# Kernel tuning notes

Measured on AMD Instinct MI355X. Metric: run time of the kernel, lower is better.

## Reference

```python
import jax, jax.numpy as jnp
import numpy as np

N, E = 100000, 1600000
IN_C, OUT_C, H, EDGE_DIM = 128, 64, 2, 4
NEG_SLOPE = 0.2
LN_EPS = 1e-5


def setup_inputs() -> dict:
    key = jax.random.key(0)
    ks = jax.random.split(key, 12)
    s = 1.0 / np.sqrt(IN_C)
    inp = {
        "x": jax.random.normal(ks[0], (N, IN_C), jnp.float32),
        "edge_index": jax.random.randint(ks[1], (2, E), 0, N, jnp.int64),
        "edge_attr": jax.random.normal(ks[2], (E, EDGE_DIM), jnp.float32),
        "W": jax.random.normal(ks[3], (IN_C, H * OUT_C), jnp.float32) * s,
        "att_src": jax.random.normal(ks[4], (H, OUT_C), jnp.float32) * s,
        "att_dst": jax.random.normal(ks[5], (H, OUT_C), jnp.float32) * s,
        "W_edge": jax.random.normal(ks[6], (EDGE_DIM, H * OUT_C), jnp.float32) * 0.5,
        "att_edge": jax.random.normal(ks[7], (H, OUT_C), jnp.float32) * s,
        "bias": jnp.zeros((OUT_C,), jnp.float32),
        "gamma": jnp.ones((OUT_C,), jnp.float32),
        "beta": jnp.zeros((OUT_C,), jnp.float32),
    }
    return inp


def reference(x, edge_index, edge_attr, W, att_src, att_dst, W_edge, att_edge, bias, gamma, beta):
    n = x.shape[0]
    src, dst = edge_index[0], edge_index[1]
    # shared src/dst linear (PyG GATConv with single input tensor)
    h = (x @ W).reshape(n, H, OUT_C)                       # [N,H,C]
    a_src = jnp.einsum("nhc,hc->nh", h, att_src)          # [N,H]
    a_dst = jnp.einsum("nhc,hc->nh", h, att_dst)          # [N,H]
    e = (edge_attr @ W_edge).reshape(-1, H, OUT_C)         # [E,H,C]
    a_edge = jnp.einsum("ehc,hc->eh", e, att_edge)        # [E,H]
    alpha = jax.nn.leaky_relu(a_src[src] + a_dst[dst] + a_edge, NEG_SLOPE)  # [E,H]
    # segment softmax over edges grouped by destination node
    amax = jax.ops.segment_max(alpha, dst, num_segments=n)
    ex = jnp.exp(alpha - amax[dst])
    denom = jax.ops.segment_sum(ex, dst, num_segments=n)
    w = ex / (denom[dst] + 1e-16)                          # [E,H]
    msg = h[src] * w[:, :, None]                           # [E,H,C]
    out = jax.ops.segment_sum(msg, dst, num_segments=n)    # [N,H,C]
    out = out.mean(axis=1) + bias                          # concat=False -> head mean
    # LayerNorm + ReLU
    mu = out.mean(-1, keepdims=True)
    var = ((out - mu) ** 2).mean(-1, keepdims=True)
    out = (out - mu) * jax.lax.rsqrt(var + LN_EPS) * gamma + beta
    return jax.nn.relu(out)
```

## Files before the change

### kernel.cpp

```cpp
#include <hip/hip_runtime.h>
#include <hip/hip_fp16.h>
#include <math.h>

#define IN_C 128
#define HC   128
#define OUT_C 64
#define NEG_SLOPE 0.2f
#define LN_EPS 1e-5f
#define CHUNK 4096
#define BSH   8
#define BMSK  255
#define NBMAX 512
#define NB2MAX 1024

typedef __attribute__((ext_vector_type(8))) short bf16x8;
typedef __attribute__((ext_vector_type(4))) float f32x4;

__device__ inline unsigned bf16pack(float a, float b) {
    unsigned ua = __float_as_uint(a), ub = __float_as_uint(b);
    ua = (ua + 0x7fffu + ((ua >> 16) & 1u)) >> 16;
    ub = (ub + 0x7fffu + ((ub >> 16) & 1u)) >> 16;
    return ua | (ub << 16);
}

__global__ __launch_bounds__(256) void k_pre(const float* __restrict__ W,
                                             const float* __restrict__ W_edge,
                                             const float* __restrict__ att_edge,
                                             const int* __restrict__ ei_dst,
                                             unsigned short* __restrict__ WbfT,
                                             float* __restrict__ V,
                                             int* __restrict__ off,
                                             int E, int NB, int PB) {
    __shared__ int hist[NBMAX];
    int b = blockIdx.x, t = threadIdx.x;
    if (b < 8) {
        #pragma unroll
        for (int i = 0; i < 8; ++i) {
            int idx = b * 2048 + i * 256 + t;
            int k = idx >> 7, col = idx & 127;
            unsigned u = __float_as_uint(W[idx]);
            WbfT[col * 128 + k] =
                (unsigned short)((u + 0x7fffu + ((u >> 16) & 1u)) >> 16);
        }
        return;
    }
    if (b == 8) {
        if (t < 8) {
            int d = t >> 1, h = t & 1;
            float s = 0.f;
            for (int c = 0; c < 64; ++c)
                s += W_edge[d * HC + h * 64 + c] * att_edge[h * 64 + c];
            V[d * 2 + h] = s;
        }
        return;
    }
    int pb = b - 9;
    for (int i = t; i < NB; i += 256) hist[i] = 0;
    __syncthreads();
    int base = pb * CHUNK;
    int lim = E - base; if (lim > CHUNK) lim = CHUNK;
    if (lim == CHUNK) {
        #pragma unroll
        for (int u = 0; u < 4; ++u) {
            int4 v = *(const int4*)&ei_dst[base + u * 1024 + t * 4];
            atomicAdd(&hist[v.x >> BSH], 1);
            atomicAdd(&hist[v.y >> BSH], 1);
            atomicAdd(&hist[v.z >> BSH], 1);
            atomicAdd(&hist[v.w >> BSH], 1);
        }
    } else {
        for (int i = t; i < lim; i += 256)
            atomicAdd(&hist[ei_dst[base + i] >> BSH], 1);
    }
    __syncthreads();
    for (int i = t; i < NB; i += 256)
        off[(size_t)i * PB + pb] = hist[i];
}

__global__ __launch_bounds__(256) void k_mid(const float* __restrict__ x,
                                             const unsigned short* __restrict__ WbfT,
                                             const float* __restrict__ attS,
                                             const float* __restrict__ attD,
                                             unsigned* __restrict__ hb,
                                             float* __restrict__ a_src,
                                             float* __restrict__ a_dst, int M,
                                             int* __restrict__ off,
                                             int* __restrict__ bsum,
                                             int nS, int GB) {
    __shared__ unsigned xb[64 * 64];
    const int t = threadIdx.x;
    const int bid = blockIdx.x;

    if (bid >= GB) {
        int* sm = (int*)xb;
        int blk = bid - GB;
        int base = blk * 1024 + t * 4;
        int v0 = 0, v1 = 0, v2 = 0, v3 = 0;
        if (base + 0 < nS) v0 = off[base + 0];
        if (base + 1 < nS) v1 = off[base + 1];
        if (base + 2 < nS) v2 = off[base + 2];
        if (base + 3 < nS) v3 = off[base + 3];
        int s = v0 + v1 + v2 + v3;
        sm[t] = s;
        __syncthreads();
        for (int o = 1; o < 256; o <<= 1) {
            int u = (t >= o) ? sm[t - o] : 0;
            __syncthreads();
            sm[t] += u;
            __syncthreads();
        }
        int excl = sm[t] - s;
        if (base + 0 < nS) off[base + 0] = excl;
        if (base + 1 < nS) off[base + 1] = excl + v0;
        if (base + 2 < nS) off[base + 2] = excl + v0 + v1;
        if (base + 3 < nS) off[base + 3] = excl + v0 + v1 + v2;
        if (t == 255) bsum[blk] = sm[255];
        return;
    }

    const int brow = bid * 64;
    const float4* x4 = (const float4*)x;
    #pragma unroll
    for (int i = 0; i < 8; ++i) {
        int idx = i * 256 + t;
        int row = idx >> 5, c4 = idx & 31;
        float4 v = make_float4(0.f, 0.f, 0.f, 0.f);
        if (brow + row < M) v = x4[(size_t)(brow + row) * 32 + c4];
        unsigned lo = bf16pack(v.x, v.y), hi = bf16pack(v.z, v.w);
        int byte = row * 256 + ((c4 * 8) ^ ((row & 7) << 4));
        *(uint2*)((char*)xb + byte) = make_uint2(lo, hi);
    }
    __syncthreads();

    const int w = t >> 6, lane = t & 63;
    const int col = lane & 15, qr = lane >> 4;
    f32x4 acc[8];
    #pragma unroll
    for (int ct = 0; ct < 8; ++ct) acc[ct] = (f32x4){0.f, 0.f, 0.f, 0.f};

    const int arow = w * 16 + col;
    #pragma unroll
    for (int ks = 0; ks < 4; ++ks) {
        int abyte = arow * 256 + ((ks * 64 + qr * 16) ^ ((arow & 7) << 4));
        bf16x8 af = *(const bf16x8*)((const char*)xb + abyte);
        #pragma unroll
        for (int ct = 0; ct < 8; ++ct) {
            bf16x8 bfr = *(const bf16x8*)&WbfT[(size_t)(ct * 16 + col) * 128 + ks * 32 + qr * 8];
            acc[ct] = __builtin_amdgcn_mfma_f32_16x16x32_bf16(af, bfr, acc[ct], 0, 0, 0);
        }
    }

    float pS0[4], pS1[4], pD0[4], pD1[4];
    #pragma unroll
    for (int r = 0; r < 4; ++r) { pS0[r] = pS1[r] = pD0[r] = pD1[r] = 0.f; }
    #pragma unroll
    for (int ct = 0; ct < 8; ++ct) {
        float s = attS[ct * 16 + col], d = attD[ct * 16 + col];
        #pragma unroll
        for (int r = 0; r < 4; ++r) {
            float a = acc[ct][r];
            if (ct < 4) { pS0[r] += a * s; pD0[r] += a * d; }
            else        { pS1[r] += a * s; pD1[r] += a * d; }
        }
    }
    #pragma unroll
    for (int m = 1; m < 16; m <<= 1) {
        #pragma unroll
        for (int r = 0; r < 4; ++r) {
            pS0[r] += __shfl_xor(pS0[r], m);
            pS1[r] += __shfl_xor(pS1[r], m);
            pD0[r] += __shfl_xor(pD0[r], m);
            pD1[r] += __shfl_xor(pD1[r], m);
        }
    }
    #pragma unroll
    for (int r = 0; r < 4; ++r) {
        int grow = brow + w * 16 + qr * 4 + r;
        if (grow < M) {
            if (col == 0) {
                a_src[2 * grow + 0] = pS0[r];
                a_src[2 * grow + 1] = pS1[r];
                a_dst[2 * grow + 0] = pD0[r];
                a_dst[2 * grow + 1] = pD1[r];
            }
            #pragma unroll
            for (int ct = 0; ct < 4; ++ct)
                hb[(size_t)grow * 64 + ct * 16 + col] =
                    bf16pack(acc[ct][r], acc[ct + 4][r]);
        }
    }
}

__device__ inline void scan_bsum(const int* __restrict__ bsum, int nb2,
                                 int* bs, int* sm, int t) {
    int v0 = (4 * t + 0 < nb2) ? bsum[4 * t + 0] : 0;
    int v1 = (4 * t + 1 < nb2) ? bsum[4 * t + 1] : 0;
    int v2 = (4 * t + 2 < nb2) ? bsum[4 * t + 2] : 0;
    int v3 = (4 * t + 3 < nb2) ? bsum[4 * t + 3] : 0;
    int s = v0 + v1 + v2 + v3;
    sm[t] = s;
    __syncthreads();
    for (int o = 1; o < 256; o <<= 1) {
        int u = (t >= o) ? sm[t - o] : 0;
        __syncthreads();
        sm[t] += u;
        __syncthreads();
    }
    int excl = sm[t] - s;
    bs[4 * t + 0] = excl;
    bs[4 * t + 1] = excl + v0;
    bs[4 * t + 2] = excl + v0 + v1;
    bs[4 * t + 3] = excl + v0 + v1 + v2;
    __syncthreads();
}

__global__ __launch_bounds__(256) void k_part(const int* __restrict__ ei,
                                              const float* __restrict__ ea,
                                              const float* __restrict__ V,
                                              const float* __restrict__ a_src,
                                              const float* __restrict__ a_dst,
                                              const int* __restrict__ off,
                                              const int* __restrict__ bsum,
                                              int* __restrict__ bsum2,
                                              uint2* __restrict__ pA,
                                              int E, int NB, int PB, int nb2) {
    __shared__ int cur[NBMAX];
    __shared__ int bs[NB2MAX];
    __shared__ int sm[256];
    int pb = blockIdx.x, t = threadIdx.x;

    scan_bsum(bsum, nb2, bs, sm, t);
    if (pb == 0)
        for (int i = t; i < nb2; i += 256) bsum2[i] = bs[i];

    for (int i = t; i < NB; i += 256) {
        size_t oi = (size_t)i * PB + pb;
        cur[i] = off[oi] + bs[(int)(oi >> 10)];
    }
    __syncthreads();
    float v0 = V[0], v1 = V[1], v2 = V[2], v3 = V[3];
    float v4 = V[4], v5 = V[5], v6 = V[6], v7 = V[7];
    int base = pb * CHUNK;
    int lim = E - base; if (lim > CHUNK) lim = CHUNK;

    if (lim == CHUNK) {
        #pragma unroll
        for (int h = 0; h < 2; ++h) {
            int e0 = base + h * 2048 + t;
            int sA[8], dA[8];
            #pragma unroll
            for (int k = 0; k < 8; ++k) {
                sA[k] = ei[e0 + k * 256];
                dA[k] = ei[E + e0 + k * 256];
            }
            float4 aA[8];
            #pragma unroll
            for (int k = 0; k < 8; ++k) aA[k] = ((const float4*)ea)[e0 + k * 256];
            float2 asA[8], adA[8];
            #pragma unroll
            for (int k = 0; k < 8; ++k) {
                asA[k] = ((const float2*)a_src)[sA[k]];
                adA[k] = ((const float2*)a_dst)[dA[k]];
            }
            #pragma unroll
            for (int k = 0; k < 8; ++k) {
                float ae0 = aA[k].x * v0 + aA[k].y * v2 + aA[k].z * v4 + aA[k].w * v6;
                float ae1 = aA[k].x * v1 + aA[k].y * v3 + aA[k].z * v5 + aA[k].w * v7;
                float al0 = asA[k].x + adA[k].x + ae0;
                al0 = al0 > 0.f ? al0 : NEG_SLOPE * al0;
                float al1 = asA[k].y + adA[k].y + ae1;
                al1 = al1 > 0.f ? al1 : NEG_SLOPE * al1;
                __half2 hx = __floats2half2_rn(__expf(al0), __expf(al1));
                int slot = atomicAdd(&cur[dA[k] >> BSH], 1);
                pA[slot] = make_uint2((unsigned)sA[k] | ((unsigned)(dA[k] & BMSK) << 17),
                                      *reinterpret_cast<unsigned*>(&hx));
            }
        }
    } else {
        for (int i = t; i < lim; i += 256) {
            int e = base + i;
            int s = ei[e], d = ei[E + e];
            float4 a = ((const float4*)ea)[e];
            float ae0 = a.x * v0 + a.y * v2 + a.z * v4 + a.w * v6;
            float ae1 = a.x * v1 + a.y * v3 + a.z * v5 + a.w * v7;
            float2 as = ((const float2*)a_src)[s];
            float2 ad = ((const float2*)a_dst)[d];
            float al0 = as.x + ad.x + ae0; al0 = al0 > 0.f ? al0 : NEG_SLOPE * al0;
            float al1 = as.y + ad.y + ae1; al1 = al1 > 0.f ? al1 : NEG_SLOPE * al1;
            __half2 hx = __floats2half2_rn(__expf(al0), __expf(al1));
            int slot = atomicAdd(&cur[d >> BSH], 1);
            pA[slot] = make_uint2((unsigned)s | ((unsigned)(d & BMSK) << 17),
                                  *reinterpret_cast<unsigned*>(&hx));
        }
    }
}

__global__ __launch_bounds__(256) void k_csr(const uint2* __restrict__ pA,
                                             const int* __restrict__ off,
                                             const int* __restrict__ bsum2,
                                             int* __restrict__ rowptr,
                                             uint2* __restrict__ payload,
                                             int M, int E, int NB, int PB) {
    __shared__ int cnt[256];
    __shared__ int sc[256];
    __shared__ int cur[256];
    int b = blockIdx.x, t = threadIdx.x;
    int n0 = b << BSH;
    int nloc = M - n0; if (nloc > 256) nloc = 256;

    size_t o0 = (size_t)b * PB;
    int s0 = off[o0] + bsum2[(int)(o0 >> 10)];
    int s1 = E;
    if (b + 1 < NB) {
        size_t o1 = (size_t)(b + 1) * PB;
        s1 = off[o1] + bsum2[(int)(o1 >> 10)];
    }
    cnt[t] = 0;
    __syncthreads();

    for (int i = s0 + t; i < s1; i += 256)
        atomicAdd(&cnt[(pA[i].x >> 17) & BMSK], 1);
    __syncthreads();
    int c = cnt[t];
    sc[t] = c;
    __syncthreads();
    for (int o = 1; o < 256; o <<= 1) {
        int u = (t >= o) ? sc[t - o] : 0;
        __syncthreads();
        sc[t] += u;
        __syncthreads();
    }
    {
        int base = s0 + sc[t] - c;
        cur[t] = base;
        if (t < nloc) rowptr[n0 + t] = base;
    }
    if (b == NB - 1 && t == 0) rowptr[M] = E;
    __syncthreads();
    for (int i = s0 + t; i < s1; i += 256) {
        uint2 p = pA[i];
        int dl = (p.x >> 17) & BMSK;
        int pos = atomicAdd(&cur[dl], 1);
        payload[pos] = make_uint2(p.x & 0x1FFFF, p.y);
    }
}

__global__ __launch_bounds__(256) void k_gather(const uint2* __restrict__ payload,
                                                const int* __restrict__ rowptr,
                                                const unsigned* __restrict__ hb,
                                                const float* __restrict__ bias,
                                                const float* __restrict__ gamma,
                                                const float* __restrict__ beta,
                                                float* __restrict__ out, int M) {
    __shared__ uint2 stg[4][64];
    int w = threadIdx.x >> 6, lane = threadIdx.x & 63;
    int n = blockIdx.x * 4 + w;
    if (n >= M) return;
    int beg = rowptr[n], end = rowptr[n + 1];
    float acc0 = 0.f, acc1 = 0.f, pe0 = 0.f, pe1 = 0.f;

    for (int base = beg; base < end; base += 64) {
        int cnt = end - base; if (cnt > 64) cnt = 64;
        uint2 p = make_uint2(0u, 0u);
        if (lane < cnt) p = payload[base + lane];
        stg[w][lane] = p;
        {
            __half2 he = *reinterpret_cast<__half2*>(&p.y);
            pe0 += __low2float(he);
            pe1 += __high2float(he);
        }
        int j = 0;
        for (; j + 8 <= cnt; j += 8) {
            uint2 q0 = stg[w][j + 0], q1 = stg[w][j + 1];
            uint2 q2 = stg[w][j + 2], q3 = stg[w][j + 3];
            uint2 q4 = stg[w][j + 4], q5 = stg[w][j + 5];
            uint2 q6 = stg[w][j + 6], q7 = stg[w][j + 7];
            int s0 = __builtin_amdgcn_readfirstlane((int)q0.x);
            int s1 = __builtin_amdgcn_readfirstlane((int)q1.x);
            int s2 = __builtin_amdgcn_readfirstlane((int)q2.x);
            int s3 = __builtin_amdgcn_readfirstlane((int)q3.x);
            int s4 = __builtin_amdgcn_readfirstlane((int)q4.x);
            int s5 = __builtin_amdgcn_readfirstlane((int)q5.x);
            int s6 = __builtin_amdgcn_readfirstlane((int)q6.x);
            int s7 = __builtin_amdgcn_readfirstlane((int)q7.x);
            unsigned h0 = (hb + (size_t)s0 * 64)[lane];
            unsigned h1 = (hb + (size_t)s1 * 64)[lane];
            unsigned h2 = (hb + (size_t)s2 * 64)[lane];
            unsigned h3 = (hb + (size_t)s3 * 64)[lane];
            unsigned h4 = (hb + (size_t)s4 * 64)[lane];
            unsigned h5 = (hb + (size_t)s5 * 64)[lane];
            unsigned h6 = (hb + (size_t)s6 * 64)[lane];
            unsigned h7 = (hb + (size_t)s7 * 64)[lane];
            __half2 e0 = *reinterpret_cast<__half2*>(&q0.y);
            __half2 e1 = *reinterpret_cast<__half2*>(&q1.y);
            __half2 e2 = *reinterpret_cast<__half2*>(&q2.y);
            __half2 e3 = *reinterpret_cast<__half2*>(&q3.y);
            __half2 e4 = *reinterpret_cast<__half2*>(&q4.y);
            __half2 e5 = *reinterpret_cast<__half2*>(&q5.y);
            __half2 e6 = *reinterpret_cast<__half2*>(&q6.y);
            __half2 e7 = *reinterpret_cast<__half2*>(&q7.y);
            acc0 += __low2float(e0)  * __uint_as_float(h0 << 16);
            acc1 += __high2float(e0) * __uint_as_float(h0 & 0xffff0000u);
            acc0 += __low2float(e1)  * __uint_as_float(h1 << 16);
            acc1 += __high2float(e1) * __uint_as_float(h1 & 0xffff0000u);
            acc0 += __low2float(e2)  * __uint_as_float(h2 << 16);
            acc1 += __high2float(e2) * __uint_as_float(h2 & 0xffff0000u);
            acc0 += __low2float(e3)  * __uint_as_float(h3 << 16);
            acc1 += __high2float(e3) * __uint_as_float(h3 & 0xffff0000u);
            acc0 += __low2float(e4)  * __uint_as_float(h4 << 16);
            acc1 += __high2float(e4) * __uint_as_float(h4 & 0xffff0000u);
            acc0 += __low2float(e5)  * __uint_as_float(h5 << 16);
            acc1 += __high2float(e5) * __uint_as_float(h5 & 0xffff0000u);
            acc0 += __low2float(e6)  * __uint_as_float(h6 << 16);
            acc1 += __high2float(e6) * __uint_as_float(h6 & 0xffff0000u);
            acc0 += __low2float(e7)  * __uint_as_float(h7 << 16);
            acc1 += __high2float(e7) * __uint_as_float(h7 & 0xffff0000u);
        }
        for (; j + 4 <= cnt; j += 4) {
            uint2 q0 = stg[w][j + 0], q1 = stg[w][j + 1];
            uint2 q2 = stg[w][j + 2], q3 = stg[w][j + 3];
            int s0 = __builtin_amdgcn_readfirstlane((int)q0.x);
            int s1 = __builtin_amdgcn_readfirstlane((int)q1.x);
            int s2 = __builtin_amdgcn_readfirstlane((int)q2.x);
            int s3 = __builtin_amdgcn_readfirstlane((int)q3.x);
            unsigned h0 = (hb + (size_t)s0 * 64)[lane];
            unsigned h1 = (hb + (size_t)s1 * 64)[lane];
            unsigned h2 = (hb + (size_t)s2 * 64)[lane];
            unsigned h3 = (hb + (size_t)s3 * 64)[lane];
            __half2 e0 = *reinterpret_cast<__half2*>(&q0.y);
            __half2 e1 = *reinterpret_cast<__half2*>(&q1.y);
            __half2 e2 = *reinterpret_cast<__half2*>(&q2.y);
            __half2 e3 = *reinterpret_cast<__half2*>(&q3.y);
            acc0 += __low2float(e0)  * __uint_as_float(h0 << 16);
            acc1 += __high2float(e0) * __uint_as_float(h0 & 0xffff0000u);
            acc0 += __low2float(e1)  * __uint_as_float(h1 << 16);
            acc1 += __high2float(e1) * __uint_as_float(h1 & 0xffff0000u);
            acc0 += __low2float(e2)  * __uint_as_float(h2 << 16);
            acc1 += __high2float(e2) * __uint_as_float(h2 & 0xffff0000u);
            acc0 += __low2float(e3)  * __uint_as_float(h3 << 16);
            acc1 += __high2float(e3) * __uint_as_float(h3 & 0xffff0000u);
        }
        for (; j < cnt; ++j) {
            uint2 q0 = stg[w][j];
            int s0 = __builtin_amdgcn_readfirstlane((int)q0.x);
            unsigned h0 = (hb + (size_t)s0 * 64)[lane];
            __half2 e0 = *reinterpret_cast<__half2*>(&q0.y);
            acc0 += __low2float(e0)  * __uint_as_float(h0 << 16);
            acc1 += __high2float(e0) * __uint_as_float(h0 & 0xffff0000u);
        }
    }

    float d0 = pe0, d1 = pe1;
    #pragma unroll
    for (int m = 32; m; m >>= 1) {
        d0 += __shfl_xor(d0, m);
        d1 += __shfl_xor(d1, m);
    }

    float o = 0.5f * (acc0 / (d0 + 1e-16f) + acc1 / (d1 + 1e-16f)) + bias[lane];
    float mu = o;
    #pragma unroll
    for (int m = 32; m; m >>= 1) mu += __shfl_xor(mu, m);
    mu *= (1.f / 64.f);
    float c = o - mu;
    float v = c * c;
    #pragma unroll
    for (int m = 32; m; m >>= 1) v += __shfl_xor(v, m);
    v *= (1.f / 64.f);
    float y = c * rsqrtf(v + LN_EPS) * gamma[lane] + beta[lane];
    out[(size_t)n * OUT_C + lane] = fmaxf(y, 0.f);
}

extern "C" void kernel_launch(void* const* d_in, const int* in_sizes, int n_in,
                              void* d_out, int out_size, void* d_ws, size_t ws_size,
                              hipStream_t stream) {
    const float* x     = (const float*)d_in[0];
    const int*   ei    = (const int*)d_in[1];
    const float* ea    = (const float*)d_in[2];
    const float* W     = (const float*)d_in[3];
    const float* attS  = (const float*)d_in[4];
    const float* attD  = (const float*)d_in[5];
    const float* We    = (const float*)d_in[6];
    const float* attE  = (const float*)d_in[7];
    const float* bias  = (const float*)d_in[8];
    const float* gamma = (const float*)d_in[9];
    const float* beta  = (const float*)d_in[10];

    const int M  = in_sizes[0] / IN_C;
    const int E  = in_sizes[1] / 2;
    const int NB = (M + BMSK) >> BSH;
    const int PB = (E + CHUNK - 1) / CHUNK;
    const int nS = NB * PB;
    const int nb2 = (nS + 1023) / 1024;
    const int GB = (M + 63) / 64;

    char* ws = (char*)d_ws;
    size_t woff = 0;
    auto alloc = [&](size_t bytes) -> void* {
        void* p = ws + woff;
        woff += (bytes + 255) & ~(size_t)255;
        return p;
    };
    unsigned*       hb     = (unsigned*)      alloc((size_t)M * 64 * 4);
    float*          a_src  = (float*)         alloc((size_t)M * 2 * 4);
    float*          a_dst  = (float*)         alloc((size_t)M * 2 * 4);
    int*            off    = (int*)           alloc((size_t)nS * 4);
    int*            bsum   = (int*)           alloc((size_t)nb2 * 4);
    int*            bsum2  = (int*)           alloc((size_t)nb2 * 4);
    int*            rowptr = (int*)           alloc((size_t)(M + 1) * 4);
    uint2*          pA     = (uint2*)         alloc((size_t)E * 8);
    uint2*          payload= (uint2*)         alloc((size_t)E * 8);
    unsigned short* WbfT   = (unsigned short*)alloc(128 * 128 * 2);
    float*          V      = (float*)         alloc(32);

    k_pre<<<9 + PB, 256, 0, stream>>>(W, We, attE, ei + E, WbfT, V, off, E, NB, PB);
    k_mid<<<GB + nb2, 256, 0, stream>>>(x, WbfT, attS, attD, hb, a_src, a_dst, M,
                                        off, bsum, nS, GB);
    k_part<<<PB, 256, 0, stream>>>(ei, ea, V, a_src, a_dst, off, bsum, bsum2,
                                   pA, E, NB, PB, nb2);
    k_csr<<<NB, 256, 0, stream>>>(pA, off, bsum2, rowptr, payload, M, E, NB, PB);
    k_gather<<<(M + 3) / 4, 256, 0, stream>>>(payload, rowptr, hb, bias, gamma, beta,
                                              (float*)d_out, M);
}
```

Measured before the change: 159.1 us.

## Overlap edge partitioning with node GEMM by deferring attention logits to CSR pass

Splits the offset scan into its own kernel and fuses the node projection GEMM with the edge partition pass into one interleaved launch, with one in five blocks partitioning edges. This lets the two independent workloads run concurrently. The attention logit and exp computation moves into the CSR build, which stores the edge term as half in the payload and gathers a_src there. The cost is an extra random gather of a_src in k_csr, a separate scan launch, and precision loss from storing the pre-activation edge logit in fp16.

Result: faster. 144.1 us (-9.5%).

```diff
diff --git a/kernel.cpp b/kernel.cpp
--- a/kernel.cpp
+++ b/kernel.cpp
@@ -77,48 +77,133 @@
         off[(size_t)i * PB + pb] = hist[i];
 }
 
-__global__ __launch_bounds__(256) void k_mid(const float* __restrict__ x,
-                                             const unsigned short* __restrict__ WbfT,
-                                             const float* __restrict__ attS,
-                                             const float* __restrict__ attD,
-                                             unsigned* __restrict__ hb,
-                                             float* __restrict__ a_src,
-                                             float* __restrict__ a_dst, int M,
-                                             int* __restrict__ off,
-                                             int* __restrict__ bsum,
-                                             int nS, int GB) {
+__global__ __launch_bounds__(256) void k_scan(int* __restrict__ off,
+                                              int* __restrict__ bsum, int nS) {
+    __shared__ int sm[256];
+    int t = threadIdx.x;
+    int base = blockIdx.x * 1024 + t * 4;
+    int v0 = 0, v1 = 0, v2 = 0, v3 = 0;
+    if (base + 0 < nS) v0 = off[base + 0];
+    if (base + 1 < nS) v1 = off[base + 1];
+    if (base + 2 < nS) v2 = off[base + 2];
+    if (base + 3 < nS) v3 = off[base + 3];
+    int s = v0 + v1 + v2 + v3;
+    sm[t] = s;
+    __syncthreads();
+    for (int o = 1; o < 256; o <<= 1) {
+        int u = (t >= o) ? sm[t - o] : 0;
+        __syncthreads();
+        sm[t] += u;
+        __syncthreads();
+    }
+    int excl = sm[t] - s;
+    if (base + 0 < nS) off[base + 0] = excl;
+    if (base + 1 < nS) off[base + 1] = excl + v0;
+    if (base + 2 < nS) off[base + 2] = excl + v0 + v1;
+    if (base + 3 < nS) off[base + 3] = excl + v0 + v1 + v2;
+    if (t == 255) bsum[blockIdx.x] = sm[255];
+}
+
+__device__ inline void scan_bsum(const int* __restrict__ bsum, int nb2,
+                                 int* bs, int* sm, int t) {
+    int v0 = (4 * t + 0 < nb2) ? bsum[4 * t + 0] : 0;
+    int v1 = (4 * t + 1 < nb2) ? bsum[4 * t + 1] : 0;
+    int v2 = (4 * t + 2 < nb2) ? bsum[4 * t + 2] : 0;
+    int v3 = (4 * t + 3 < nb2) ? bsum[4 * t + 3] : 0;
+    int s = v0 + v1 + v2 + v3;
+    sm[t] = s;
+    __syncthreads();
+    for (int o = 1; o < 256; o <<= 1) {
+        int u = (t >= o) ? sm[t - o] : 0;
+        __syncthreads();
+        sm[t] += u;
+        __syncthreads();
+    }
+    int excl = sm[t] - s;
+    bs[4 * t + 0] = excl;
+    bs[4 * t + 1] = excl + v0;
+    bs[4 * t + 2] = excl + v0 + v1;
+    bs[4 * t + 3] = excl + v0 + v1 + v2;
+    __syncthreads();
+}
+
+__global__ __launch_bounds__(256) void k_fused(
+        const float* __restrict__ x,
+        const unsigned short* __restrict__ WbfT,
+        const float* __restrict__ attS, const float* __restrict__ attD,
+        unsigned* __restrict__ hb,
+        float* __restrict__ a_src, float* __restrict__ a_dst, int M,
+        const int* __restrict__ ei, const float* __restrict__ ea,
+        const float* __restrict__ V,
+        const int* __restrict__ off, const int* __restrict__ bsum,
+        int* __restrict__ bsum2, uint2* __restrict__ pA,
+        int E, int NB, int PB, int nb2, int GB) {
     __shared__ unsigned xb[64 * 64];
     const int t = threadIdx.x;
     const int bid = blockIdx.x;
-
-    if (bid >= GB) {
-        int* sm = (int*)xb;
-        int blk = bid - GB;
-        int base = blk * 1024 + t * 4;
-        int v0 = 0, v1 = 0, v2 = 0, v3 = 0;
-        if (base + 0 < nS) v0 = off[base + 0];
-        if (base + 1 < nS) v1 = off[base + 1];
-        if (base + 2 < nS) v2 = off[base + 2];
-        if (base + 3 < nS) v3 = off[base + 3];
-        int s = v0 + v1 + v2 + v3;
-        sm[t] = s;
-        __syncthreads();
-        for (int o = 1; o < 256; o <<= 1) {
-            int u = (t >= o) ? sm[t - o] : 0;
-            __syncthreads();
-            sm[t] += u;
-            __syncthreads();
-        }
-        int excl = sm[t] - s;
-        if (base + 0 < nS) off[base + 0] = excl;
-        if (base + 1 < nS) off[base + 1] = excl + v0;
-        if (base + 2 < nS) off[base + 2] = excl + v0 + v1;
-        if (base + 3 < nS) off[base + 3] = excl + v0 + v1 + v2;
-        if (t == 255) bsum[blk] = sm[255];
+    const int r5 = bid % 5, g5 = bid / 5;
+
+    if (r5 == 4) {
+        int* cur = (int*)xb;
+        int* bs  = (int*)xb + NBMAX;
+        int* sm  = (int*)xb + NBMAX + NB2MAX;
+        int pb = g5;
+        scan_bsum(bsum, nb2, bs, sm, t);
+        if (pb == 0)
+            for (int i = t; i < nb2; i += 256) bsum2[i] = bs[i];
+        for (int i = t; i < NB; i += 256) {
+            size_t oi = (size_t)i * PB + pb;
+            cur[i] = off[oi] + bs[(int)(oi >> 10)];
+        }
+        __syncthreads();
+        float v0 = V[0], v1 = V[1], v2 = V[2], v3 = V[3];
+        float v4 = V[4], v5 = V[5], v6 = V[6], v7 = V[7];
+        int base = pb * CHUNK;
+        int lim = E - base; if (lim > CHUNK) lim = CHUNK;
+        if (lim == CHUNK) {
+            #pragma unroll
+            for (int h = 0; h < 2; ++h) {
+                int e0 = base + h * 2048 + t;
+                int sA[8], dA[8];
+                #pragma unroll
+                for (int k = 0; k < 8; ++k) {
+                    sA[k] = ei[e0 + k * 256];
+                    dA[k] = ei[E + e0 + k * 256];
+                }
+                float4 aA[8];
+                #pragma unroll
+                for (int k = 0; k < 8; ++k)
+                    aA[k] = ((const float4*)ea)[e0 + k * 256];
+                #pragma unroll
+                for (int k = 0; k < 8; ++k) {
+                    float ae0 = aA[k].x * v0 + aA[k].y * v2 + aA[k].z * v4 + aA[k].w * v6;
+                    float ae1 = aA[k].x * v1 + aA[k].y * v3 + aA[k].z * v5 + aA[k].w * v7;
+                    __half2 hx = __floats2half2_rn(ae0, ae1);
+                    int slot = atomicAdd(&cur[dA[k] >> BSH], 1);
+                    pA[slot] = make_uint2(
+                        (unsigned)sA[k] | ((unsigned)(dA[k] & BMSK) << 17),
+                        *reinterpret_cast<unsigned*>(&hx));
+                }
+            }
+        } else {
+            for (int i = t; i < lim; i += 256) {
+                int e = base + i;
+                int s = ei[e], d = ei[E + e];
+                float4 a = ((const float4*)ea)[e];
+                float ae0 = a.x * v0 + a.y * v2 + a.z * v4 + a.w * v6;
+                float ae1 = a.x * v1 + a.y * v3 + a.z * v5 + a.w * v7;
+                __half2 hx = __floats2half2_rn(ae0, ae1);
+                int slot = atomicAdd(&cur[d >> BSH], 1);
+                pA[slot] = make_uint2((unsigned)s | ((unsigned)(d & BMSK) << 17),
+                                      *reinterpret_cast<unsigned*>(&hx));
+            }
+        }
         return;
     }
 
-    const int brow = bid * 64;
+    const int gid = g5 * 4 + r5;
+    if (gid >= GB) return;
+    const int brow = gid * 64;
     const float4* x4 = (const float4*)x;
     #pragma unroll
     for (int i = 0; i < 8; ++i) {
@@ -191,119 +276,18 @@
     }
 }
 
-__device__ inline void scan_bsum(const int* __restrict__ bsum, int nb2,
-                                 int* bs, int* sm, int t) {
-    int v0 = (4 * t + 0 < nb2) ? bsum[4 * t + 0] : 0;
-    int v1 = (4 * t + 1 < nb2) ? bsum[4 * t + 1] : 0;
-    int v2 = (4 * t + 2 < nb2) ? bsum[4 * t + 2] : 0;
-    int v3 = (4 * t + 3 < nb2) ? bsum[4 * t + 3] : 0;
-    int s = v0 + v1 + v2 + v3;
-    sm[t] = s;
-    __syncthreads();
-    for (int o = 1; o < 256; o <<= 1) {
-        int u = (t >= o) ? sm[t - o] : 0;
-        __syncthreads();
-        sm[t] += u;
-        __syncthreads();
-    }
-    int excl = sm[t] - s;
-    bs[4 * t + 0] = excl;
-    bs[4 * t + 1] = excl + v0;
-    bs[4 * t + 2] = excl + v0 + v1;
-    bs[4 * t + 3] = excl + v0 + v1 + v2;
-    __syncthreads();
-}
-
-__global__ __launch_bounds__(256) void k_part(const int* __restrict__ ei,
-                                              const float* __restrict__ ea,
-                                              const float* __restrict__ V,
-                                              const float* __restrict__ a_src,
-                                              const float* __restrict__ a_dst,
-                                              const int* __restrict__ off,
-                                              const int* __restrict__ bsum,
-                                              int* __restrict__ bsum2,
-                                              uint2* __restrict__ pA,
-                                              int E, int NB, int PB, int nb2) {
-    __shared__ int cur[NBMAX];
-    __shared__ int bs[NB2MAX];
-    __shared__ int sm[256];
-    int pb = blockIdx.x, t = threadIdx.x;
-
-    scan_bsum(bsum, nb2, bs, sm, t);
-    if (pb == 0)
-        for (int i = t; i < nb2; i += 256) bsum2[i] = bs[i];
-
-    for (int i = t; i < NB; i += 256) {
-        size_t oi = (size_t)i * PB + pb;
-        cur[i] = off[oi] + bs[(int)(oi >> 10)];
-    }
-    __syncthreads();
-    float v0 = V[0], v1 = V[1], v2 = V[2], v3 = V[3];
-    float v4 = V[4], v5 = V[5], v6 = V[6], v7 = V[7];
-    int base = pb * CHUNK;
-    int lim = E - base; if (lim > CHUNK) lim = CHUNK;
-
-    if (lim == CHUNK) {
-        #pragma unroll
-        for (int h = 0; h < 2; ++h) {
-            int e0 = base + h * 2048 + t;
-            int sA[8], dA[8];
-            #pragma unroll
-            for (int k = 0; k < 8; ++k) {
-                sA[k] = ei[e0 + k * 256];
-                dA[k] = ei[E + e0 + k * 256];
-            }
-            float4 aA[8];
-            #pragma unroll
-            for (int k = 0; k < 8; ++k) aA[k] = ((const float4*)ea)[e0 + k * 256];
-            float2 asA[8], adA[8];
-            #pragma unroll
-            for (int k = 0; k < 8; ++k) {
-                asA[k] = ((const float2*)a_src)[sA[k]];
-                adA[k] = ((const float2*)a_dst)[dA[k]];
-            }
-            #pragma unroll
-            for (int k = 0; k < 8; ++k) {
-                float ae0 = aA[k].x * v0 + aA[k].y * v2 + aA[k].z * v4 + aA[k].w * v6;
-                float ae1 = aA[k].x * v1 + aA[k].y * v3 + aA[k].z * v5 + aA[k].w * v7;
-                float al0 = asA[k].x + adA[k].x + ae0;
-                al0 = al0 > 0.f ? al0 : NEG_SLOPE * al0;
-                float al1 = asA[k].y + adA[k].y + ae1;
-                al1 = al1 > 0.f ? al1 : NEG_SLOPE * al1;
-                __half2 hx = __floats2half2_rn(__expf(al0), __expf(al1));
-                int slot = atomicAdd(&cur[dA[k] >> BSH], 1);
-                pA[slot] = make_uint2((unsigned)sA[k] | ((unsigned)(dA[k] & BMSK) << 17),
-                                      *reinterpret_cast<unsigned*>(&hx));
-            }
-        }
-    } else {
-        for (int i = t; i < lim; i += 256) {
-            int e = base + i;
-            int s = ei[e], d = ei[E + e];
-            float4 a = ((const float4*)ea)[e];
-            float ae0 = a.x * v0 + a.y * v2 + a.z * v4 + a.w * v6;
-            float ae1 = a.x * v1 + a.y * v3 + a.z * v5 + a.w * v7;
-            float2 as = ((const float2*)a_src)[s];
-            float2 ad = ((const float2*)a_dst)[d];
-            float al0 = as.x + ad.x + ae0; al0 = al0 > 0.f ? al0 : NEG_SLOPE * al0;
-            float al1 = as.y + ad.y + ae1; al1 = al1 > 0.f ? al1 : NEG_SLOPE * al1;
-            __half2 hx = __floats2half2_rn(__expf(al0), __expf(al1));
-            int slot = atomicAdd(&cur[d >> BSH], 1);
-            pA[slot] = make_uint2((unsigned)s | ((unsigned)(d & BMSK) << 17),
-                                  *reinterpret_cast<unsigned*>(&hx));
-        }
-    }
-}
-
 __global__ __launch_bounds__(256) void k_csr(const uint2* __restrict__ pA,
                                              const int* __restrict__ off,
                                              const int* __restrict__ bsum2,
+                                             const float* __restrict__ a_src,
+                                             const float* __restrict__ a_dst,
                                              int* __restrict__ rowptr,
                                              uint2* __restrict__ payload,
                                              int M, int E, int NB, int PB) {
     __shared__ int cnt[256];
     __shared__ int sc[256];
     __shared__ int cur[256];
+    __shared__ float2 adl[256];
     int b = blockIdx.x, t = threadIdx.x;
     int n0 = b << BSH;
     int nloc = M - n0; if (nloc > 256) nloc = 256;
@@ -316,6 +300,7 @@
         s1 = off[o1] + bsum2[(int)(o1 >> 10)];
     }
     cnt[t] = 0;
+    if (t < nloc) adl[t] = ((const float2*)a_dst)[n0 + t];
     __syncthreads();
 
     for (int i = s0 + t; i < s1; i += 256)
@@ -339,9 +324,18 @@
     __syncthreads();
     for (int i = s0 + t; i < s1; i += 256) {
         uint2 p = pA[i];
+        int src = p.x & 0x1FFFF;
         int dl = (p.x >> 17) & BMSK;
+        __half2 aeh = *reinterpret_cast<__half2*>(&p.y);
+        float2 as = ((const float2*)a_src)[src];
+        float2 ad = adl[dl];
+        float al0 = as.x + ad.x + __low2float(aeh);
+        al0 = al0 > 0.f ? al0 : NEG_SLOPE * al0;
+        float al1 = as.y + ad.y + __high2float(aeh);
+        al1 = al1 > 0.f ? al1 : NEG_SLOPE * al1;
+        __half2 hx = __floats2half2_rn(__expf(al0), __expf(al1));
         int pos = atomicAdd(&cur[dl], 1);
-        payload[pos] = make_uint2(p.x & 0x1FFFF, p.y);
+        payload[pos] = make_uint2((unsigned)src, *reinterpret_cast<unsigned*>(&hx));
     }
 }
 
@@ -514,11 +508,12 @@
     float*          V      = (float*)         alloc(32);
 
     k_pre<<<9 + PB, 256, 0, stream>>>(W, We, attE, ei + E, WbfT, V, off, E, NB, PB);
-    k_mid<<<GB + nb2, 256, 0, stream>>>(x, WbfT, attS, attD, hb, a_src, a_dst, M,
-                                        off, bsum, nS, GB);
-    k_part<<<PB, 256, 0, stream>>>(ei, ea, V, a_src, a_dst, off, bsum, bsum2,
-                                   pA, E, NB, PB, nb2);
-    k_csr<<<NB, 256, 0, stream>>>(pA, off, bsum2, rowptr, payload, M, E, NB, PB);
+    k_scan<<<nb2, 256, 0, stream>>>(off, bsum, nS);
+    k_fused<<<5 * PB, 256, 0, stream>>>(x, WbfT, attS, attD, hb, a_src, a_dst, M,
+                                        ei, ea, V, off, bsum, bsum2, pA,
+                                        E, NB, PB, nb2, GB);
+    k_csr<<<NB, 256, 0, stream>>>(pA, off, bsum2, a_src, a_dst, rowptr, payload,
+                                  M, E, NB, PB);
     k_gather<<<(M + 3) / 4, 256, 0, stream>>>(payload, rowptr, hb, bias, gamma, beta,
                                               (float*)d_out, M);
 }
```
